# Kernel optimization log

Measured on AMD Instinct MI355X. Metric: run time of the kernel, lower is better.

## Reference

```python
import jax, jax.numpy as jnp
import numpy as np


def setup_inputs() -> dict:
    key = jax.random.key(0)
    ks = jax.random.split(key, 14)
    B, Ld, Lq, D = 64, 512, 128, 512
    d_node = jax.random.normal(ks[0], (B, Ld, D), jnp.float32)
    q_node = jax.random.normal(ks[1], (B, Lq, D), jnp.float32)
    qq_graph = jax.random.randint(ks[2], (B, Lq, Lq), 0, 2, jnp.int32)
    dq_graph = jax.random.randint(ks[3], (B, Ld, Lq), 0, 2, jnp.int32)
    dd_graph = jax.random.randint(ks[4], (B, Ld, Ld), 0, 2, jnp.int32)
    qd_graph = jax.random.randint(ks[5], (B, Lq, Ld), 0, 2, jnp.int32)
    s = 0.02
    W_nw = jax.random.normal(ks[6], (1, D), jnp.float32) * s
    b_nw = jnp.zeros((1,), jnp.float32)
    W_self = jax.random.normal(ks[7], (D, D), jnp.float32) * s
    b_self = jnp.zeros((D,), jnp.float32)
    W_dd = jax.random.normal(ks[8], (D, D), jnp.float32) * s
    W_qq = jax.random.normal(ks[9], (D, D), jnp.float32) * s
    W_dq = jax.random.normal(ks[10], (D, D), jnp.float32) * s
    W_qd = jax.random.normal(ks[11], (D, D), jnp.float32) * s
    return {"d_node": d_node, "q_node": q_node, "qq_graph": qq_graph,
            "dq_graph": dq_graph, "dd_graph": dd_graph, "qd_graph": qd_graph,
            "W_nw": W_nw, "b_nw": b_nw, "W_self": W_self, "b_self": b_self,
            "W_dd": W_dd, "W_qq": W_qq, "W_dq": W_dq, "W_qd": W_qd,
            "iteration_steps": 2}


def reference(d_node, q_node, qq_graph, dq_graph, dd_graph, qd_graph,
              W_nw, b_nw, W_self, b_self, W_dd, W_qq, W_dq, W_qd,
              iteration_steps):
    dd = dd_graph.astype(jnp.float32)
    dq = dq_graph.astype(jnp.float32)
    qq = qq_graph.astype(jnp.float32)
    qd = qd_graph.astype(jnp.float32)

    # neighbor counts, clamped to 1 where a node has no neighbors
    d_nb = dd.sum(-1) + dq.sum(-1)              # [B, Ld]
    d_nb = jnp.where(d_nb >= 1.0, d_nb, 1.0)
    q_nb = qq.sum(-1) + qd.sum(-1)              # [B, Lq]
    q_nb = jnp.where(q_nb >= 1.0, q_nb, 1.0)

    all_d_w, all_q_w = [], []
    for _ in range(iteration_steps):
        d_w = jax.nn.sigmoid(jnp.einsum('bld,od->blo', d_node, W_nw) + b_nw)[..., 0]  # [B, Ld]
        q_w = jax.nn.sigmoid(jnp.einsum('bld,od->blo', q_node, W_nw) + b_nw)[..., 0]  # [B, Lq]
        all_d_w.append(d_w)
        all_q_w.append(q_w)

        self_d = jnp.einsum('bld,od->blo', d_node, W_self) + b_self
        self_q = jnp.einsum('bld,od->blo', q_node, W_self) + b_self
        dd_info = jnp.einsum('bld,od->blo', d_node, W_dd)
        qd_info = jnp.einsum('bld,od->blo', d_node, W_qd)
        qq_info = jnp.einsum('bld,od->blo', q_node, W_qq)
        dq_info = jnp.einsum('bld,od->blo', q_node, W_dq)

        # masked weights: graph is 0/1, so replace_masked_values(., graph, 0) == graph * weight
        dd_msg = jnp.einsum('bij,bjd->bid', dd * d_w[:, None, :], dd_info)  # [B,Ld,D]
        qd_msg = jnp.einsum('bij,bjd->bid', qd * d_w[:, None, :], qd_info)  # [B,Lq,D]
        qq_msg = jnp.einsum('bij,bjd->bid', qq * q_w[:, None, :], qq_info)  # [B,Lq,D]
        dq_msg = jnp.einsum('bij,bjd->bid', dq * q_w[:, None, :], dq_info)  # [B,Ld,D]

        agg_q = (qq_msg + qd_msg) / q_nb[..., None]
        agg_d = (dd_msg + dq_msg) / d_nb[..., None]
        d_node = jax.nn.relu(self_d + agg_d)
        q_node = jax.nn.relu(self_q + agg_q)

    all_d_w = jnp.stack(all_d_w, axis=1)  # [B, steps, Ld]
    all_q_w = jnp.stack(all_q_w, axis=1)  # [B, steps, Lq]
    return (d_node, q_node, all_d_w, all_q_w)
```

## Files before the change

kernel.cpp:

```cpp
#include <hip/hip_runtime.h>
#include <cstdint>
#include <cstddef>

typedef _Float16 h16;
typedef __attribute__((ext_vector_type(8))) _Float16 h16x8;
typedef __attribute__((ext_vector_type(4))) _Float16 h16x4;
typedef __attribute__((ext_vector_type(4))) float f32x4;

constexpr int B_ = 64, LD = 512, LQ = 128, DIM = 512, STEPS = 2;
constexpr int MD = B_ * LD;
constexpr int MQ = B_ * LQ;
constexpr int KST = LD + LQ;
constexpr int KAGG = KST + DIM;

#define ASYNC16(gp, lp)                                                          \
  __builtin_amdgcn_global_load_lds(                                              \
      (const __attribute__((address_space(1))) unsigned int*)(gp),               \
      (__attribute__((address_space(3))) unsigned int*)(lp), 16, 0, 0)

struct Src {
  const h16* p0; int s0; long bstr0;
  const h16* p1; int s1; long bstr1;
  int ksplit;
};

template <int WM, class Epi>
__device__ __forceinline__ void gemm_body(int b, long tileM, long tileN,
                                          Src sa, Src sb, int K,
                                          const Epi& epi, h16* lds) {
  constexpr int BM = WM * 32;
  constexpr int AS = BM / 64;
  constexpr int AE = BM * 32;
  constexpr int BUFE = AE + 4096;

  const int tid = threadIdx.x;
  const int lane = tid & 63;
  const int wv = tid >> 6;
  const int wi = wv >> 1, wj = wv & 1;
  const int quad = lane >> 4, l16 = lane & 15;

  const int r = tid >> 2;
  const int es = (r ^ (r >> 2)) & 3;
  const int kq = (tid & 3) ^ es;

  const h16* pa[2][AS];
  const h16* pb[2][2];
#pragma unroll
  for (int s = 0; s < AS; s++) {
    pa[0][s] = sa.p0 + (size_t)b * sa.bstr0 + (tileM + r + 64 * s) * (long)sa.s0 + kq * 8;
    pa[1][s] = sa.p1 + (size_t)b * sa.bstr1 + (tileM + r + 64 * s) * (long)sa.s1 + kq * 8 - sa.ksplit;
  }
#pragma unroll
  for (int s = 0; s < 2; s++) {
    pb[0][s] = sb.p0 + (size_t)b * sb.bstr0 + (tileN + r + 64 * s) * (long)sb.s0 + kq * 8;
    pb[1][s] = sb.p1 + (size_t)b * sb.bstr1 + (tileN + r + 64 * s) * (long)sb.s1 + kq * 8 - sb.ksplit;
  }

  const int ef = (l16 ^ (l16 >> 2)) & 3;
  int offA[WM], offB[4];
#pragma unroll
  for (int i = 0; i < WM; i++) {
    const int row = wi * WM * 16 + i * 16 + l16;
    offA[i] = (row * 4 + (quad ^ ef)) * 8;
  }
#pragma unroll
  for (int j = 0; j < 4; j++) {
    const int row = wj * 64 + j * 16 + l16;
    offB[j] = AE + (row * 4 + (quad ^ ef)) * 8;
  }

  f32x4 acc[WM][4] = {};
  const int T = K >> 5;

  auto dmaTile = [&](int t, int c) {
    const int k0 = t * 32;
    h16* base = lds + c * BUFE + tid * 8;
    const int sel = (k0 >= sa.ksplit);
#pragma unroll
    for (int s = 0; s < AS; s++) ASYNC16(pa[sel][s] + k0, base + s * 2048);
    const int selb = (k0 >= sb.ksplit);
#pragma unroll
    for (int s = 0; s < 2; s++) ASYNC16(pb[selb][s] + k0, base + AE + s * 2048);
  };
  auto mfmaStep = [&](int off) {
    h16x8 af[WM], bf[4];
#pragma unroll
    for (int i = 0; i < WM; i++) af[i] = *(const h16x8*)(lds + off + offA[i]);
#pragma unroll
    for (int j = 0; j < 4; j++) bf[j] = *(const h16x8*)(lds + off + offB[j]);
#pragma unroll
    for (int i = 0; i < WM; i++)
#pragma unroll
      for (int j = 0; j < 4; j++)
        acc[i][j] = __builtin_amdgcn_mfma_f32_16x16x32_f16(af[i], bf[j], acc[i][j], 0, 0, 0);
  };

  dmaTile(0, 0);

  for (int t = 0; t < T; t += 2) {
    __syncthreads();
    dmaTile(t + 1, 1);
    mfmaStep(0);
    __syncthreads();
    if (t + 2 < T) dmaTile(t + 2, 0);
    mfmaStep(BUFE);
  }

#pragma unroll
  for (int i = 0; i < WM; i++) {
#pragma unroll
    for (int j = 0; j < 4; j++) {
      const int gm0 = (int)tileM + wi * WM * 16 + i * 16 + quad * 4;
      const int gn  = (int)tileN + wj * 64 + j * 16 + l16;
#pragma unroll
      for (int rr = 0; rr < 4; rr++) epi(b, gm0 + rr, gn, acc[i][j][rr]);
    }
  }
}

struct EpiDense {
  const float* w;
  h16* stackA;
  h16* stackB;
  int lnShift;
  int offA, offB;
  __device__ void operator()(int, int gm, int gn, float v) const {
    const int b = gn >> lnShift, l = gn & ((1 << lnShift) - 1);
    const h16 sv = (h16)(w[gn] * v);
    if (gm < 512)
      stackA[((size_t)b * 512 + gm) * 640 + offA + l] = sv;
    else
      stackB[((size_t)b * 512 + (gm - 512)) * 640 + offB + l] = sv;
  }
};
struct EpiAgg {
  const float* bias;
  float* out;
  h16* nodeNext;
  int rowsPerB;
  __device__ void operator()(int b, int gm, int gn, float v) const {
    const size_t row = (size_t)b * rowsPerB + gm;
    const float val = fmaxf(v + bias[gn], 0.f);
    if (out) out[row * 512 + gn] = val;
    nodeNext[row * 512 + gn] = (h16)val;
  }
};

__global__ __launch_bounds__(256, 2) void k_dense(Src saD, Src sbD, EpiDense epiD,
                                                  Src saQ, Src sbQ, EpiDense epiQ) {
  __shared__ __align__(16) h16 lds[2 * (256 * 32 + 128 * 32)];
  const int g = blockIdx.x;
  const int x = g / 320;
  const int yy = g % 320;
  if (yy < 256)
    gemm_body<8>(0, (long)x * 256, (long)yy * 128, saD, sbD, 512, epiD, lds);
  else
    gemm_body<8>(0, (long)x * 256, (long)(yy - 256) * 128, saQ, sbQ, 512, epiQ, lds);
}

__global__ __launch_bounds__(256, 2) void k_agg(Src saD, Src sbD, EpiAgg epiD,
                                                Src saQ, Src sbQ, EpiAgg epiQ) {
  __shared__ __align__(16) h16 lds[2 * (256 * 32 + 128 * 32)];
  const int g = blockIdx.x;
  const int b = g & 63;
  const int inner = g >> 6;
  if (inner < 8)
    gemm_body<8>(b, (long)(inner >> 2) * 256, (long)(inner & 3) * 128, saD, sbD, KAGG, epiD, lds);
  else
    gemm_body<4>(b, 0L, (long)(inner - 8) * 128, saQ, sbQ, KAGG, epiQ, lds);
}

__global__ __launch_bounds__(256) void k_convert(const float* __restrict__ dn,
                                                 const float* __restrict__ qn,
                                                 h16* __restrict__ dnb,
                                                 h16* __restrict__ qnb) {
  const size_t i4 = ((size_t)blockIdx.x * 256 + threadIdx.x) * 4;
  constexpr size_t TD = (size_t)MD * DIM;
  const float* src; h16* dst; size_t idx;
  if (i4 < TD) { src = dn; dst = dnb; idx = i4; }
  else         { src = qn; dst = qnb; idx = i4 - TD; }
  const float4 v = *(const float4*)&src[idx];
  h16x4 o; o.x = (h16)v.x; o.y = (h16)v.y; o.z = (h16)v.z; o.w = (h16)v.w;
  *(h16x4*)&dst[idx] = o;
}

__global__ __launch_bounds__(256) void k_wcat(const float* __restrict__ Wself,
                                              const float* __restrict__ Wdd,
                                              const float* __restrict__ Wqd,
                                              const float* __restrict__ Wqq,
                                              const float* __restrict__ Wdq,
                                              h16* __restrict__ catD,
                                              h16* __restrict__ catQ) {
  const int i = blockIdx.x * 256 + threadIdx.x;
  float vD, vQ;
  if (i < 512 * 512)       { vD = Wself[i];            vQ = vD; }
  else if (i < 1024 * 512) { vD = Wdd[i - 512 * 512];  vQ = Wqq[i - 512 * 512]; }
  else                     { vD = Wqd[i - 1024 * 512]; vQ = Wdq[i - 1024 * 512]; }
  catD[i] = (h16)vD; catQ[i] = (h16)vQ;
}

__global__ __launch_bounds__(256) void k_maskD(const int* __restrict__ dd,
                                               const int* __restrict__ dq,
                                               h16* __restrict__ maskD) {
  const int row = blockIdx.x * 4 + (threadIdx.x >> 6);
  const int lane = threadIdx.x & 63;
  const int* pdd = dd + (size_t)row * 512;
  const int* pdq = dq + (size_t)row * 128;
  h16* pm = maskD + (size_t)row * 640;
  float vals[10];
  float s = 0.f;
#pragma unroll
  for (int t = 0; t < 10; t++) {
    const int j = lane + t * 64;
    const float v = (float)((j < 512) ? pdd[j] : pdq[j - 512]);
    vals[t] = v; s += v;
  }
  for (int m = 32; m; m >>= 1) s += __shfl_xor(s, m);
  const float inv = 1.f / fmaxf(s, 1.f);
#pragma unroll
  for (int t = 0; t < 10; t++) pm[lane + t * 64] = (h16)(vals[t] * inv);
}

__global__ __launch_bounds__(256) void k_maskQ(const int* __restrict__ qq,
                                               const int* __restrict__ qd,
                                               h16* __restrict__ maskQ) {
  const int row = blockIdx.x * 4 + (threadIdx.x >> 6);
  const int lane = threadIdx.x & 63;
  const int* pqq = qq + (size_t)row * 128;
  const int* pqd = qd + (size_t)row * 512;
  h16* pm = maskQ + (size_t)row * 640;
  float vals[10];
  float s = 0.f;
#pragma unroll
  for (int t = 0; t < 10; t++) {
    const int j = lane + t * 64;
    const float v = (float)((j < 128) ? pqq[j] : pqd[j - 128]);
    vals[t] = v; s += v;
  }
  for (int m = 32; m; m >>= 1) s += __shfl_xor(s, m);
  const float inv = 1.f / fmaxf(s, 1.f);
#pragma unroll
  for (int t = 0; t < 10; t++) pm[lane + t * 64] = (h16)(vals[t] * inv);
}

__global__ __launch_bounds__(256) void k_w(const h16* __restrict__ dnb,
                                           const h16* __restrict__ qnb,
                                           const float* __restrict__ Wnw,
                                           const float* __restrict__ bnw,
                                           float* __restrict__ d_w,
                                           float* __restrict__ q_w,
                                           float* __restrict__ adw,
                                           float* __restrict__ aqw, int it) {
  const int row = blockIdx.x * 4 + (threadIdx.x >> 6);
  const int lane = threadIdx.x & 63;
  const bool isD = row < MD;
  const h16* node = isD ? dnb + (size_t)row * 512 : qnb + (size_t)(row - MD) * 512;
  const h16x8 v = *(const h16x8*)&node[lane * 8];
  const float4 w0 = *(const float4*)&Wnw[lane * 8];
  const float4 w1 = *(const float4*)&Wnw[lane * 8 + 4];
  float s = (float)v[0] * w0.x + (float)v[1] * w0.y + (float)v[2] * w0.z +
            (float)v[3] * w0.w + (float)v[4] * w1.x + (float)v[5] * w1.y +
            (float)v[6] * w1.z + (float)v[7] * w1.w;
  for (int m = 32; m; m >>= 1) s += __shfl_xor(s, m);
  if (lane == 0) {
    const float w = 1.f / (1.f + expf(-(s + bnw[0])));
    if (isD) {
      d_w[row] = w;
      adw[((size_t)(row >> 9) * STEPS + it) * 512 + (row & 511)] = w;
    } else {
      const int rq = row - MD;
      q_w[rq] = w;
      aqw[((size_t)(rq >> 7) * STEPS + it) * 128 + (rq & 127)] = w;
    }
  }
}

extern "C" void kernel_launch(void* const* d_in, const int* in_sizes, int n_in,
                              void* d_out, int out_size, void* d_ws, size_t ws_size,
                              hipStream_t stream) {
  (void)in_sizes; (void)n_in; (void)out_size; (void)ws_size;

  const float* d_node = (const float*)d_in[0];
  const float* q_node = (const float*)d_in[1];
  const int*   qq     = (const int*)d_in[2];
  const int*   dq     = (const int*)d_in[3];
  const int*   dd     = (const int*)d_in[4];
  const int*   qd     = (const int*)d_in[5];
  const float* W_nw   = (const float*)d_in[6];
  const float* b_nw   = (const float*)d_in[7];
  const float* W_self = (const float*)d_in[8];
  const float* b_self = (const float*)d_in[9];
  const float* W_dd   = (const float*)d_in[10];
  const float* W_qq   = (const float*)d_in[11];
  const float* W_dq   = (const float*)d_in[12];
  const float* W_qd   = (const float*)d_in[13];

  float* outd = (float*)d_out;
  float* outq = outd + (size_t)MD * DIM;
  float* adw  = outq + (size_t)MQ * DIM;
  float* aqw  = adw + (size_t)B_ * STEPS * LD;

  char* p = (char*)d_ws;
  auto alloc = [&](size_t bytes) { char* r = p; p += (bytes + 255) & ~(size_t)255; return r; };
  h16* dnode[2], *qnode[2];
  dnode[0] = (h16*)alloc((size_t)MD * DIM * 2);
  dnode[1] = (h16*)alloc((size_t)MD * DIM * 2);
  qnode[0] = (h16*)alloc((size_t)MQ * DIM * 2);
  qnode[1] = (h16*)alloc((size_t)MQ * DIM * 2);
  h16* catD    = (h16*)alloc((size_t)1536 * 512 * 2);
  h16* catQ    = (h16*)alloc((size_t)1536 * 512 * 2);
  h16* maskD   = (h16*)alloc((size_t)B_ * LD * KST * 2);
  h16* maskQ   = (h16*)alloc((size_t)B_ * LQ * KST * 2);
  h16* stackDT = (h16*)alloc((size_t)B_ * 512 * KST * 2);
  h16* stackQT = (h16*)alloc((size_t)B_ * 512 * KST * 2);
  float* d_wb  = (float*)alloc((size_t)MD * 4);
  float* q_wb  = (float*)alloc((size_t)MQ * 4);

  k_convert<<<dim3((MD * DIM + MQ * DIM) / 4 / 256), 256, 0, stream>>>(d_node, q_node, dnode[0], qnode[0]);
  k_wcat<<<dim3(1536 * 512 / 256), 256, 0, stream>>>(W_self, W_dd, W_qd, W_qq, W_dq, catD, catQ);
  k_maskD<<<dim3(MD / 4), 256, 0, stream>>>(dd, dq, maskD);
  k_maskQ<<<dim3(MQ / 4), 256, 0, stream>>>(qq, qd, maskQ);

  for (int it = 0; it < STEPS; it++) {
    const bool last = (it == STEPS - 1);
    h16* ncur_d = dnode[it & 1];
    h16* nnext_d = dnode[(it & 1) ^ 1];
    h16* ncur_q = qnode[it & 1];
    h16* nnext_q = qnode[(it & 1) ^ 1];

    k_w<<<dim3((MD + MQ) / 4), 256, 0, stream>>>(ncur_d, ncur_q, W_nw, b_nw, d_wb, q_wb, adw, aqw, it);

    {
      Src saD{catD + 512 * 512, 512, 0, catD + 512 * 512, 512, 0, 512};
      Src sbD{ncur_d, 512, 0, ncur_d, 512, 0, 512};
      Src saQ{catQ + 512 * 512, 512, 0, catQ + 512 * 512, 512, 0, 512};
      Src sbQ{ncur_q, 512, 0, ncur_q, 512, 0, 512};
      k_dense<<<dim3(1280), 256, 0, stream>>>(
          saD, sbD, EpiDense{d_wb, stackDT, stackQT, 9, 0, 128},
          saQ, sbQ, EpiDense{q_wb, stackQT, stackDT, 7, 0, 512});
    }
    {
      Src saD{maskD, 640, (long)LD * KST, ncur_d, 512, (long)LD * DIM, KST};
      Src sbD{stackDT, 640, (long)512 * KST, catD, 512, 0, KST};
      Src saQ{maskQ, 640, (long)LQ * KST, ncur_q, 512, (long)LQ * DIM, KST};
      Src sbQ{stackQT, 640, (long)512 * KST, catQ, 512, 0, KST};
      k_agg<<<dim3(768), 256, 0, stream>>>(
          saD, sbD, EpiAgg{b_self, last ? outd : nullptr, nnext_d, 512},
          saQ, sbQ, EpiAgg{b_self, last ? outq : nullptr, nnext_q, 128});
    }
  }
}
```

Before: 567.3 us.

## Triple-buffer GEMM LDS pipeline with vmcnt waits and single barrier per tile

Replaces the double-buffered K loop, which used two barriers per pair of tiles, with a three-stage LDS ring. Loads run two tiles ahead, and a partial s_waitcnt vmcnt plus one barrier guards each tile, so global-to-LDS DMA overlaps more with MFMA work. It also skips writing the fp16 next-node buffer on the last iteration and reorders k_agg blocks so the smaller Q tiles launch first. LDS use grows by half, which may lower occupancy. The hard-coded vmcnt counts must match the number of async loads issued per tile.

```diff
diff --git a/kernel.cpp b/kernel.cpp
--- a/kernel.cpp
+++ b/kernel.cpp
@@ -72,9 +72,9 @@
   f32x4 acc[WM][4] = {};
   const int T = K >> 5;
 
-  auto dmaTile = [&](int t, int c) {
+  auto dmaTile = [&](int t, int off) {
     const int k0 = t * 32;
-    h16* base = lds + c * BUFE + tid * 8;
+    h16* base = lds + off + tid * 8;
     const int sel = (k0 >= sa.ksplit);
 #pragma unroll
     for (int s = 0; s < AS; s++) ASYNC16(pa[sel][s] + k0, base + s * 2048);
@@ -96,15 +96,26 @@
   };
 
   dmaTile(0, 0);
-
-  for (int t = 0; t < T; t += 2) {
-    __syncthreads();
-    dmaTile(t + 1, 1);
-    mfmaStep(0);
-    __syncthreads();
-    if (t + 2 < T) dmaTile(t + 2, 0);
-    mfmaStep(BUFE);
-  }
+  dmaTile(1, BUFE);
+
+  int co = 0;
+  int no = 2 * BUFE;
+  for (int t = 0; t < T - 1; ++t) {
+    if constexpr (WM == 8) asm volatile("s_waitcnt vmcnt(6)" ::: "memory");
+    else                   asm volatile("s_waitcnt vmcnt(4)" ::: "memory");
+    __builtin_amdgcn_s_barrier();
+    asm volatile("" ::: "memory");
+    __builtin_amdgcn_sched_barrier(0);
+    if (t + 2 < T) dmaTile(t + 2, no);
+    mfmaStep(co);
+    co = (co == 2 * BUFE) ? 0 : co + BUFE;
+    no = (no == 2 * BUFE) ? 0 : no + BUFE;
+  }
+  asm volatile("s_waitcnt vmcnt(0)" ::: "memory");
+  __builtin_amdgcn_s_barrier();
+  asm volatile("" ::: "memory");
+  __builtin_amdgcn_sched_barrier(0);
+  mfmaStep(co);
 
 #pragma unroll
   for (int i = 0; i < WM; i++) {
@@ -142,13 +153,13 @@
     const size_t row = (size_t)b * rowsPerB + gm;
     const float val = fmaxf(v + bias[gn], 0.f);
     if (out) out[row * 512 + gn] = val;
-    nodeNext[row * 512 + gn] = (h16)val;
+    if (nodeNext) nodeNext[row * 512 + gn] = (h16)val;
   }
 };
 
 __global__ __launch_bounds__(256, 2) void k_dense(Src saD, Src sbD, EpiDense epiD,
                                                   Src saQ, Src sbQ, EpiDense epiQ) {
-  __shared__ __align__(16) h16 lds[2 * (256 * 32 + 128 * 32)];
+  __shared__ __align__(16) h16 lds[3 * (256 * 32 + 128 * 32)];
   const int g = blockIdx.x;
   const int x = g / 320;
   const int yy = g % 320;
@@ -160,14 +171,16 @@
 
 __global__ __launch_bounds__(256, 2) void k_agg(Src saD, Src sbD, EpiAgg epiD,
                                                 Src saQ, Src sbQ, EpiAgg epiQ) {
-  __shared__ __align__(16) h16 lds[2 * (256 * 32 + 128 * 32)];
+  __shared__ __align__(16) h16 lds[3 * (256 * 32 + 128 * 32)];
   const int g = blockIdx.x;
   const int b = g & 63;
   const int inner = g >> 6;
-  if (inner < 8)
-    gemm_body<8>(b, (long)(inner >> 2) * 256, (long)(inner & 3) * 128, saD, sbD, KAGG, epiD, lds);
-  else
-    gemm_body<4>(b, 0L, (long)(inner - 8) * 128, saQ, sbQ, KAGG, epiQ, lds);
+  if (inner >= 4) {
+    const int i2 = inner - 4;
+    gemm_body<8>(b, (long)(i2 >> 2) * 256, (long)(i2 & 3) * 128, saD, sbD, KAGG, epiD, lds);
+  } else {
+    gemm_body<4>(b, 0L, (long)inner * 128, saQ, sbQ, KAGG, epiQ, lds);
+  }
 }
 
 __global__ __launch_bounds__(256) void k_convert(const float* __restrict__ dn,
@@ -345,8 +358,8 @@
       Src saQ{maskQ, 640, (long)LQ * KST, ncur_q, 512, (long)LQ * DIM, KST};
       Src sbQ{stackQT, 640, (long)512 * KST, catQ, 512, 0, KST};
       k_agg<<<dim3(768), 256, 0, stream>>>(
-          saD, sbD, EpiAgg{b_self, last ? outd : nullptr, nnext_d, 512},
-          saQ, sbQ, EpiAgg{b_self, last ? outq : nullptr, nnext_q, 128});
+          saD, sbD, EpiAgg{b_self, last ? outd : nullptr, last ? nullptr : nnext_d, 512},
+          saQ, sbQ, EpiAgg{b_self, last ? outq : nullptr, last ? nullptr : nnext_q, 128});
     }
   }
 }
```

Measured after the change: 568.5 us. Within noise of the previous version (+0.2%).
